# Kernel optimization log

Hardware: AMD Instinct MI355X
Metric: run time of the kernel (lower is better)

The kernel has to match this reference:

```python
import jax, jax.numpy as jnp
import numpy as np

D = 1024      # d_model
H = 16        # n_heads
DH = 64       # d_head
K = 4         # conv_kernel
C = H * DH    # channels for depthwise convs


def setup_inputs() -> dict:
    key = jax.random.key(0)
    ks = jax.random.split(key, 16)
    s = 0.02
    w = lambda k, shape: (jax.random.normal(k, shape, jnp.float32) * s)
    return {
        'hidden_states': jax.random.normal(ks[0], (4, 2048, D), jnp.float32),
        'Wq': w(ks[1], (C, D)),
        'Wk': w(ks[2], (C, D)),
        'Wv': w(ks[3], (C, D)),
        'Wa': w(ks[4], (H, D)), 'ba': jnp.zeros((H,), jnp.float32),
        'Wb': w(ks[5], (H, D)), 'bb': jnp.zeros((H,), jnp.float32),
        'conv_q_w': w(ks[6], (C, 1, K)), 'conv_q_b': jnp.zeros((C,), jnp.float32),
        'conv_k_w': w(ks[7], (C, 1, K)), 'conv_k_b': jnp.zeros((C,), jnp.float32),
        'conv_v_w': w(ks[8], (C, 1, K)), 'conv_v_b': jnp.zeros((C,), jnp.float32),
        'Wg': w(ks[9], (C, D)), 'bg': jnp.zeros((C,), jnp.float32),
        'Wo': w(ks[10], (D, C)),
    }


def _causal_conv(x, w, b):
    # x: (B, C, T); depthwise causal conv (torch pads K-1 both sides then slices [:T])
    y = jax.lax.conv_general_dilated(
        x, w, window_strides=(1,), padding=[(K - 1, 0)],
        feature_group_count=C, dimension_numbers=('NCH', 'OIH', 'NCH'))
    return y + b[None, :, None]


def reference(hidden_states, Wq, Wk, Wv, Wa, ba, Wb, bb,
              conv_q_w, conv_q_b, conv_k_w, conv_k_b, conv_v_w, conv_v_b,
              Wg, bg, Wo):
    B, T, _ = hidden_states.shape
    # projections -> (B, C, T) for conv
    q = jnp.einsum('btd,cd->bct', hidden_states, Wq)
    k = jnp.einsum('btd,cd->bct', hidden_states, Wk)
    v = jnp.einsum('btd,cd->bct', hidden_states, Wv)
    q = jax.nn.silu(_causal_conv(q, conv_q_w, conv_q_b))
    k = jax.nn.silu(_causal_conv(k, conv_k_w, conv_k_b))
    v = jax.nn.silu(_causal_conv(v, conv_v_w, conv_v_b))
    # (B, T, H, DH)
    q = q.transpose(0, 2, 1).reshape(B, T, H, DH)
    k = k.transpose(0, 2, 1).reshape(B, T, H, DH)
    v = v.transpose(0, 2, 1).reshape(B, T, H, DH)
    # F.normalize(k, p=2, dim=-1)
    k = k / jnp.maximum(jnp.linalg.norm(k, axis=-1, keepdims=True), 1e-12)
    alpha = jax.nn.sigmoid(jnp.einsum('btd,hd->bth', hidden_states, Wa) + ba)
    beta = jax.nn.sigmoid(jnp.einsum('btd,hd->bth', hidden_states, Wb) + bb)

    def step(S, xs):
        kt, vt, qt, at, bt = xs            # (B,H,DH) x3, (B,H) x2
        v_old = jnp.einsum('bhij,bhj->bhi', S, kt)
        upd = vt - at[..., None] * v_old   # (B,H,DH)
        dS = upd[..., :, None] * kt[..., None, :]
        S = jnp.clip(at[..., None, None] * S + bt[..., None, None] * dS, -5.0, 5.0)
        ot = jnp.einsum('bhij,bhj->bhi', S, qt)
        return S, ot

    S0 = jnp.zeros((B, H, DH, DH), hidden_states.dtype)
    xs = (k.transpose(1, 0, 2, 3), v.transpose(1, 0, 2, 3), q.transpose(1, 0, 2, 3),
          alpha.transpose(1, 0, 2), beta.transpose(1, 0, 2))
    _, ys = jax.lax.scan(step, S0, xs)     # ys: (T, B, H, DH)
    y = ys.transpose(1, 0, 2, 3).reshape(B, T, C)
    g = jax.nn.silu(jnp.einsum('btd,cd->btc', hidden_states, Wg) + bg)
    y = y * g
    out = jnp.einsum('btc,dc->btd', y, Wo)
    return out
```

## Files before the change

kernel.cpp:

```cpp
#include <hip/hip_runtime.h>
#include <cstdint>
#include <cstddef>

#define TSEQ 2048
#define NB   4
#define NH   16
#define MM   (NB * TSEQ)
#define KK   1024
#define NCAT 4224

typedef __attribute__((ext_vector_type(8))) __bf16 bf16x8;
typedef __attribute__((ext_vector_type(4))) float f32x4;
typedef __attribute__((ext_vector_type(4))) int   int4v;

__device__ __forceinline__ unsigned short f2bf(float f) {
  unsigned int u = __float_as_uint(f);
  u += 0x7fffu + ((u >> 16) & 1u);
  return (unsigned short)(u >> 16);
}
__device__ __forceinline__ float bf2f(unsigned short h) {
  return __uint_as_float(((unsigned int)h) << 16);
}
__device__ __forceinline__ float sigmoidf_(float x) { return 1.0f / (1.0f + expf(-x)); }
__device__ __forceinline__ float siluf_(float x)    { return x / (1.0f + expf(-x)); }

__device__ __forceinline__ uint32_t packsplit(float x) {
  unsigned short h = f2bf(x);
  unsigned short l = f2bf(x - bf2f(h));
  return ((uint32_t)h << 16) | (uint32_t)l;
}

union BF8 { bf16x8 v; unsigned short s[8]; };

__device__ __forceinline__ void frag_from_packed(const uint32_t* p, bf16x8& hi, bf16x8& lo) {
  int4v a = *(const int4v*)p;
  int4v b = *(const int4v*)(p + 4);
  BF8 H, L;
#pragma unroll
  for (int e = 0; e < 4; ++e) {
    uint32_t ua = ((const uint32_t*)&a)[e];
    uint32_t ub = ((const uint32_t*)&b)[e];
    H.s[e]     = (unsigned short)(ua >> 16);
    L.s[e]     = (unsigned short)(ua & 0xffffu);
    H.s[e + 4] = (unsigned short)(ub >> 16);
    L.s[e + 4] = (unsigned short)(ub & 0xffffu);
  }
  hi = H.v; lo = L.v;
}

__device__ __forceinline__ f32x4 mfma3(bf16x8 ah, bf16x8 al, bf16x8 bh, bf16x8 bl, f32x4 acc) {
  acc = __builtin_amdgcn_mfma_f32_16x16x32_bf16(ah, bh, acc, 0, 0, 0);
  acc = __builtin_amdgcn_mfma_f32_16x16x32_bf16(ah, bl, acc, 0, 0, 0);
  acc = __builtin_amdgcn_mfma_f32_16x16x32_bf16(al, bh, acc, 0, 0, 0);
  return acc;
}

__global__ void k_split(const float* __restrict__ x, unsigned short* __restrict__ hi,
                        unsigned short* __restrict__ lo, int n) {
  int idx = blockIdx.x * blockDim.x + threadIdx.x;
  if (idx >= n) return;
  float v = x[idx];
  unsigned short h = f2bf(v);
  hi[idx] = h;
  lo[idx] = f2bf(v - bf2f(h));
}

__global__ void k_build_wcat(const float* __restrict__ Wq, const float* __restrict__ Wk,
                             const float* __restrict__ Wv, const float* __restrict__ Wg,
                             const float* __restrict__ Wa, const float* __restrict__ Wb,
                             unsigned short* __restrict__ hi, unsigned short* __restrict__ lo) {
  int idx = blockIdx.x * blockDim.x + threadIdx.x;
  if (idx >= NCAT * KK) return;
  int row = idx >> 10, col = idx & 1023;
  float v = 0.0f;
  if      (row < 1024) v = Wq[idx];
  else if (row < 2048) v = Wk[idx - 1024 * 1024];
  else if (row < 3072) v = Wv[idx - 2048 * 1024];
  else if (row < 4096) v = Wg[idx - 3072 * 1024];
  else if (row < 4112) v = Wa[(row - 4096) * 1024 + col];
  else if (row < 4128) v = Wb[(row - 4112) * 1024 + col];
  unsigned short h = f2bf(v);
  hi[idx] = h;
  lo[idx] = f2bf(v - bf2f(h));
}

__global__ __launch_bounds__(256, 2)
void k_gemm(const unsigned short* __restrict__ Ahi, const unsigned short* __restrict__ Alo,
            const unsigned short* __restrict__ Bhi, const unsigned short* __restrict__ Blo,
            int Kdim, int mode,
            float* __restrict__ Qb, float* __restrict__ Kb, float* __restrict__ Vb,
            float* __restrict__ Gb, float* __restrict__ Ab, float* __restrict__ Bbuf,
            const float* __restrict__ bg, const float* __restrict__ ba, const float* __restrict__ bb,
            float* __restrict__ Out) {
  __shared__ __align__(16) unsigned short As_hi[128 * 32];
  __shared__ __align__(16) unsigned short As_lo[128 * 32];
  __shared__ __align__(16) unsigned short Bs_hi[128 * 32];
  __shared__ __align__(16) unsigned short Bs_lo[128 * 32];

  const int tid  = threadIdx.x;
  const int lane = tid & 63;
  const int l15  = lane & 15;
  const int quad = lane >> 4;
  const int wid  = tid >> 6;
  const int wm   = (wid >> 1) * 64;
  const int wn   = (wid & 1) * 64;
  const int m0   = blockIdx.x * 128;
  const int n0   = blockIdx.y * 128;
  const int srow = tid >> 2;
  const int skc  = (tid & 3) * 8;

  f32x4 acc[4][4];
  f32x4 zero4 = {0.f, 0.f, 0.f, 0.f};
#pragma unroll
  for (int i = 0; i < 4; ++i)
#pragma unroll
    for (int j = 0; j < 4; ++j) acc[i][j] = zero4;

  const unsigned short* pa0 = Ahi + (size_t)(m0 + srow) * Kdim + skc;
  const unsigned short* pa1 = Ahi + (size_t)(m0 + srow + 64) * Kdim + skc;
  const unsigned short* pa2 = Alo + (size_t)(m0 + srow) * Kdim + skc;
  const unsigned short* pa3 = Alo + (size_t)(m0 + srow + 64) * Kdim + skc;
  const unsigned short* pb0 = Bhi + (size_t)(n0 + srow) * Kdim + skc;
  const unsigned short* pb1 = Bhi + (size_t)(n0 + srow + 64) * Kdim + skc;
  const unsigned short* pb2 = Blo + (size_t)(n0 + srow) * Kdim + skc;
  const unsigned short* pb3 = Blo + (size_t)(n0 + srow + 64) * Kdim + skc;

  for (int kt = 0; kt < Kdim; kt += 32) {
    int4v va0 = *(const int4v*)(pa0 + kt);
    int4v va1 = *(const int4v*)(pa1 + kt);
    int4v va2 = *(const int4v*)(pa2 + kt);
    int4v va3 = *(const int4v*)(pa3 + kt);
    int4v vb0 = *(const int4v*)(pb0 + kt);
    int4v vb1 = *(const int4v*)(pb1 + kt);
    int4v vb2 = *(const int4v*)(pb2 + kt);
    int4v vb3 = *(const int4v*)(pb3 + kt);
    __syncthreads();
    *(int4v*)&As_hi[srow * 32 + skc]        = va0;
    *(int4v*)&As_hi[(srow + 64) * 32 + skc] = va1;
    *(int4v*)&As_lo[srow * 32 + skc]        = va2;
    *(int4v*)&As_lo[(srow + 64) * 32 + skc] = va3;
    *(int4v*)&Bs_hi[srow * 32 + skc]        = vb0;
    *(int4v*)&Bs_hi[(srow + 64) * 32 + skc] = vb1;
    *(int4v*)&Bs_lo[srow * 32 + skc]        = vb2;
    *(int4v*)&Bs_lo[(srow + 64) * 32 + skc] = vb3;
    __syncthreads();

    bf16x8 ah[4], al[4], bh[4], bl[4];
#pragma unroll
    for (int f = 0; f < 4; ++f) {
      int ra = (wm + f * 16 + l15) * 32 + quad * 8;
      ah[f] = *(const bf16x8*)&As_hi[ra];
      al[f] = *(const bf16x8*)&As_lo[ra];
      int rb = (wn + f * 16 + l15) * 32 + quad * 8;
      bh[f] = *(const bf16x8*)&Bs_hi[rb];
      bl[f] = *(const bf16x8*)&Bs_lo[rb];
    }
#pragma unroll
    for (int mf = 0; mf < 4; ++mf)
#pragma unroll
      for (int nf = 0; nf < 4; ++nf) {
        acc[mf][nf] = __builtin_amdgcn_mfma_f32_16x16x32_bf16(ah[mf], bh[nf], acc[mf][nf], 0, 0, 0);
        acc[mf][nf] = __builtin_amdgcn_mfma_f32_16x16x32_bf16(ah[mf], bl[nf], acc[mf][nf], 0, 0, 0);
        acc[mf][nf] = __builtin_amdgcn_mfma_f32_16x16x32_bf16(al[mf], bh[nf], acc[mf][nf], 0, 0, 0);
      }
  }

#pragma unroll
  for (int mf = 0; mf < 4; ++mf) {
    int rowb = m0 + wm + mf * 16 + quad * 4;
#pragma unroll
    for (int nf = 0; nf < 4; ++nf) {
      int col = n0 + wn + nf * 16 + l15;
      f32x4 v = acc[mf][nf];
      if (mode == 1) {
#pragma unroll
        for (int r = 0; r < 4; ++r) Out[(size_t)(rowb + r) * 1024 + col] = v[r];
      } else {
        if (col < 1024) {
#pragma unroll
          for (int r = 0; r < 4; ++r) Qb[(size_t)(rowb + r) * 1024 + col] = v[r];
        } else if (col < 2048) {
          int c = col - 1024;
#pragma unroll
          for (int r = 0; r < 4; ++r) Kb[(size_t)(rowb + r) * 1024 + c] = v[r];
        } else if (col < 3072) {
          int c = col - 2048;
#pragma unroll
          for (int r = 0; r < 4; ++r) Vb[(size_t)(rowb + r) * 1024 + c] = v[r];
        } else if (col < 4096) {
          int c = col - 3072;
          float bgc = bg[c];
#pragma unroll
          for (int r = 0; r < 4; ++r) {
            float x = v[r] + bgc;
            Gb[(size_t)(rowb + r) * 1024 + c] = siluf_(x);
          }
        } else if (col < 4112) {
          int c = col - 4096;
          float bac = ba[c];
#pragma unroll
          for (int r = 0; r < 4; ++r) Ab[(size_t)(rowb + r) * 16 + c] = sigmoidf_(v[r] + bac);
        } else if (col < 4128) {
          int c = col - 4112;
          float bbc = bb[c];
#pragma unroll
          for (int r = 0; r < 4; ++r) Bbuf[(size_t)(rowb + r) * 16 + c] = sigmoidf_(v[r] + bbc);
        }
      }
    }
  }
}

__global__ __launch_bounds__(512)
void k_intra(const float* __restrict__ Qb, const float* __restrict__ Kb,
             const float* __restrict__ Vb,
             const float* __restrict__ Ab, const float* __restrict__ Bb,
             const float* __restrict__ cqw, const float* __restrict__ cqb,
             const float* __restrict__ ckw, const float* __restrict__ ckb,
             const float* __restrict__ cvw, const float* __restrict__ cvb,
             uint32_t* __restrict__ A1buf, unsigned short* __restrict__ Qefbuf,
             unsigned short* __restrict__ G1buf, unsigned short* __restrict__ G2Tbuf,
             float* __restrict__ gCbuf) {
  __shared__ __align__(16) unsigned short Khi[64][72], Klo[64][72];
  __shared__ __align__(16) unsigned short Qhi[64][72], Qlo[64][72];
  __shared__ float Vf[64][65];
  __shared__ float Rf[64][65];
  __shared__ float Mm[64][68];
  __shared__ __align__(16) unsigned short Atthi[64][72];
  __shared__ __align__(16) uint32_t u0T[64][68], RTp[64][68];
  __shared__ __align__(16) unsigned short KwThi[64][72], KwTlo[64][72];
  __shared__ float lgs[64], gas[64], bss[64], wvs[64], ins[64];

  const int tid  = threadIdx.x;
  const int lane = tid & 63;
  const int w8   = tid >> 6;
  const int ws   = w8 & 3;
  const int hs   = w8 >> 2;
  const int l15  = lane & 15;
  const int quad = lane >> 4;
  const int bid  = blockIdx.x;
  const int c    = bid & 31;
  const int h    = (bid >> 5) & 15;
  const int b    = bid >> 9;
  const size_t ci = (size_t)bid;
  const int t0   = c * 64;
  const long rowBase = (long)b * 2048 + t0;
  const int ch   = h * 64 + lane;
  const f32x4 z4 = {0.f, 0.f, 0.f, 0.f};

  {
    long gr = (rowBase + lane) * 16 + h;
    float av = Ab[gr], bv = Bb[gr];
    float x = log2f(av);
#pragma unroll
    for (int off = 1; off < 64; off <<= 1) {
      float y = __shfl_up(x, off);
      if (lane >= off) x += y;
    }
    float l63 = __shfl(x, 63);
    lgs[lane] = x;
    gas[lane] = exp2f(x);
    bss[lane] = bv;
    wvs[lane] = exp2f(l63 - x) * bv;
  }

  {
    const float kc0 = ckw[ch * 4], kc1 = ckw[ch * 4 + 1], kc2 = ckw[ch * 4 + 2], kc3 = ckw[ch * 4 + 3], kcbv = ckb[ch];
    const float qc0 = cqw[ch * 4], qc1 = cqw[ch * 4 + 1], qc2 = cqw[ch * 4 + 2], qc3 = cqw[ch * 4 + 3], qcbv = cqb[ch];
    const float vc0 = cvw[ch * 4], vc1 = cvw[ch * 4 + 1], vc2 = cvw[ch * 4 + 2], vc3 = cvw[ch * 4 + 3], vcbv = cvb[ch];
    const int tb = t0 + w8 * 8;
    float kw0, kw1, kw2, qw0, qw1, qw2, vw0, vw1, vw2;
    {
      float kx[3], qx[3], vx[3];
#pragma unroll
      for (int d = 0; d < 3; ++d) {
        int tt = tb - 3 + d;
        float a = 0.f, bq = 0.f, cv = 0.f;
        if (tt >= 0) {
          long ro = ((long)b * 2048 + tt) * 1024 + ch;
          a = Kb[ro]; bq = Qb[ro]; cv = Vb[ro];
        }
        kx[d] = a; qx[d] = bq; vx[d] = cv;
      }
      kw0 = kx[0]; kw1 = kx[1]; kw2 = kx[2];
      qw0 = qx[0]; qw1 = qx[1]; qw2 = qx[2];
      vw0 = vx[0]; vw1 = vx[1]; vw2 = vx[2];
    }
#pragma unroll
    for (int lt = 0; lt < 8; ++lt) {
      const int s = w8 * 8 + lt;
      const long ro = (rowBase + s) * 1024 + ch;
      float kr = Kb[ro], qr = Qb[ro], vr = Vb[ro];
      float kcv = kcbv + kc0 * kw0 + kc1 * kw1 + kc2 * kw2 + kc3 * kr;
      float qcv = qcbv + qc0 * qw0 + qc1 * qw1 + qc2 * qw2 + qc3 * qr;
      float vcv = vcbv + vc0 * vw0 + vc1 * vw1 + vc2 * vw2 + vc3 * vr;
      kw0 = kw1; kw1 = kw2; kw2 = kr;
      qw0 = qw1; qw1 = qw2; qw2 = qr;
      vw0 = vw1; vw1 = vw2; vw2 = vr;
      float kv = siluf_(kcv), qv = siluf_(qcv), vv = siluf_(vcv);
      uint32_t kp_ = packsplit(kv);
      uint32_t qp_ = packsplit(qv);
      Khi[s][lane] = (unsigned short)(kp_ >> 16); Klo[s][lane] = (unsigned short)(kp_ & 0xffffu);
      Qhi[s][lane] = (unsigned short)(qp_ >> 16); Qlo[s][lane] = (unsigned short)(qp_ & 0xffffu);
      Vf[s][lane] = vv;
    }
  }
  __syncthreads();

  f32x4 accT[4];
#pragma unroll
  for (int nt = 0; nt < 4; ++nt) accT[nt] = z4;
#pragma unroll
  for (int ks = 0; ks < 2; ++ks) {
    bf16x8 ah, al;
    if (hs == 0) {
      ah = *(const bf16x8*)&Khi[ws * 16 + l15][ks * 32 + quad * 8];
      al = *(const bf16x8*)&Klo[ws * 16 + l15][ks * 32 + quad * 8];
    } else {
      ah = *(const bf16x8*)&Qhi[ws * 16 + l15][ks * 32 + quad * 8];
      al = *(const bf16x8*)&Qlo[ws * 16 + l15][ks * 32 + quad * 8];
    }
#pragma unroll
    for (int nt = 0; nt < 4; ++nt) {
      bf16x8 bh = *(const bf16x8*)&Khi[nt * 16 + l15][ks * 32 + quad * 8];
      bf16x8 bl = *(const bf16x8*)&Klo[nt * 16 + l15][ks * 32 + quad * 8];
      accT[nt] = mfma3(ah, al, bh, bl, accT[nt]);
    }
  }
  if (hs == 0) {
#pragma unroll
    for (int nt = 0; nt < 4; ++nt)
      if (nt == ws) {
#pragma unroll
        for (int r = 0; r < 4; ++r)
          if (l15 == quad * 4 + r) ins[nt * 16 + l15] = rsqrtf(fmaxf(accT[nt][r], 1e-24f));
      }
  }
  __syncthreads();

  {
    if (hs == 0) {
#pragma unroll
      for (int nt = 0; nt < 4; ++nt) {
        int sc = nt * 16 + l15;
        float insc = ins[sc], lgc = lgs[sc], bsc = bss[sc];
#pragma unroll
        for (int r = 0; r < 4; ++r) {
          int sr = ws * 16 + quad * 4 + r;
          Mm[sr][sc] = (sc < sr) ? exp2f(lgs[sr] - lgc) * bsc * ins[sr] * insc * accT[nt][r] : 0.f;
        }
      }
    } else {
#pragma unroll
      for (int nt = 0; nt < 4; ++nt) {
        int sc = nt * 16 + l15;
        float insc = ins[sc], lgc = lgs[sc], bsc = bss[sc];
#pragma unroll
        for (int r = 0; r < 4; ++r) {
          int sr = ws * 16 + quad * 4 + r;
          Atthi[sr][sc] = f2bf((sc <= sr) ? exp2f(lgs[sr] - lgc) * bsc * insc * accT[nt][r] : 0.f);
        }
      }
    }
    int s = w8 * 8 + (lane & 7);
    int jb = (lane >> 3) * 8;
    float rsc = gas[s] * ins[s];
    float wsc = wvs[s] * ins[s];
    BF8 H0, L0;
    H0.v = *(const bf16x8*)&Khi[s][jb];
    L0.v = *(const bf16x8*)&Klo[s][jb];
#pragma unroll
    for (int e = 0; e < 8; ++e) {
      float kv = bf2f(H0.s[e]) + bf2f(L0.s[e]);
      Rf[s][jb + e] = kv * rsc;
      uint32_t p0 = packsplit(kv * wsc);
      KwThi[jb + e][s] = (unsigned short)(p0 >> 16);
      KwTlo[jb + e][s] = (unsigned short)(p0 & 0xffffu);
    }
  }
  if (tid == 0) gCbuf[ci] = gas[63];
  __syncthreads();

  if (w8 < 2) {
    float* RHS = (w8 == 0) ? &Vf[0][0] : &Rf[0][0];
    const int i = lane;
    float u[64];
#pragma unroll
    for (int d = 0; d < 4; ++d) {
      const int base = d * 16;
#pragma unroll
      for (int r2 = 0; r2 < 16; ++r2) {
        const int s = base + r2;
        float acc = RHS[s * 65 + i];
#pragma unroll
        for (int r = 0; r < r2; ++r) acc = fmaf(-Mm[s][base + r], u[base + r], acc);
        u[s] = acc;
        RHS[s * 65 + i] = acc;
      }
      if (d < 3) {
#pragma unroll 1
        for (int s = base + 16; s < 64; ++s) {
          f32x4 m0 = *(const f32x4*)&Mm[s][base];
          f32x4 m1 = *(const f32x4*)&Mm[s][base + 4];
          f32x4 m2 = *(const f32x4*)&Mm[s][base + 8];
          f32x4 m3 = *(const f32x4*)&Mm[s][base + 12];
          float a0 = m0[0] * u[base + 0] + m0[1] * u[base + 1] + m0[2] * u[base + 2] + m0[3] * u[base + 3];
          float a1 = m1[0] * u[base + 4] + m1[1] * u[base + 5] + m1[2] * u[base + 6] + m1[3] * u[base + 7];
          float a2 = m2[0] * u[base + 8] + m2[1] * u[base + 9] + m2[2] * u[base + 10] + m2[3] * u[base + 11];
          float a3 = m3[0] * u[base + 12] + m3[1] * u[base + 13] + m3[2] * u[base + 14] + m3[3] * u[base + 15];
          RHS[s * 65 + i] = RHS[s * 65 + i] - ((a0 + a1) + (a2 + a3));
        }
      }
    }
  }
  __syncthreads();

#pragma unroll
  for (int r = 0; r < 8; ++r) {
    int i = w8 * 8 + r;
    u0T[i][lane] = packsplit(Vf[lane][i]);
    RTp[i][lane] = packsplit(Rf[lane][i]);
  }
  __syncthreads();

  if (hs == 0) {
    {
      f32x4 acc[4];
#pragma unroll
      for (int nt = 0; nt < 4; ++nt) acc[nt] = z4;
#pragma unroll
      for (int ks = 0; ks < 2; ++ks) {
        bf16x8 ta = *(const bf16x8*)&Atthi[ws * 16 + l15][ks * 32 + quad * 8];
#pragma unroll
        for (int nt = 0; nt < 4; ++nt) {
          bf16x8 uh, ul;
          frag_from_packed(&u0T[nt * 16 + l15][ks * 32 + quad * 8], uh, ul);
          acc[nt] = __builtin_amdgcn_mfma_f32_16x16x32_bf16(ta, uh, acc[nt], 0, 0, 0);
          acc[nt] = __builtin_amdgcn_mfma_f32_16x16x32_bf16(ta, ul, acc[nt], 0, 0, 0);
        }
      }
#pragma unroll
      for (int nt = 0; nt < 4; ++nt)
#pragma unroll
        for (int r = 0; r < 4; ++r) {
          int t = ws * 16 + quad * 4 + r, i = nt * 16 + l15;
          A1buf[ci * 4096 + t * 64 + i] = packsplit(acc[nt][r]);
        }
    }
    {
      f32x4 acc[4];
#pragma unroll
      for (int nt = 0; nt < 4; ++nt) acc[nt] = z4;
#pragma unroll
      for (int ks = 0; ks < 2; ++ks) {
        bf16x8 ta = *(const bf16x8*)&Atthi[ws * 16 + l15][ks * 32 + quad * 8];
#pragma unroll
        for (int nt = 0; nt < 4; ++nt) {
          bf16x8 rh, rl;
          frag_from_packed(&RTp[nt * 16 + l15][ks * 32 + quad * 8], rh, rl);
          acc[nt] = __builtin_amdgcn_mfma_f32_16x16x32_bf16(ta, rh, acc[nt], 0, 0, 0);
          acc[nt] = __builtin_amdgcn_mfma_f32_16x16x32_bf16(ta, rl, acc[nt], 0, 0, 0);
        }
      }
#pragma unroll
      for (int nt = 0; nt < 4; ++nt)
#pragma unroll
        for (int r = 0; r < 4; ++r) {
          int t = ws * 16 + quad * 4 + r, j = nt * 16 + l15;
          float q = bf2f(Qhi[t][j]) + bf2f(Qlo[t][j]);
          Qefbuf[ci * 4096 + t * 64 + j] = f2bf(gas[t] * q - acc[nt][r]);
        }
    }
  } else {
    {
      f32x4 acc[4];
#pragma unroll
      for (int nt = 0; nt < 4; ++nt) acc[nt] = z4;
#pragma unroll
      for (int ks = 0; ks < 2; ++ks) {
        bf16x8 uh, ul;
        frag_from_packed(&u0T[ws * 16 + l15][ks * 32 + quad * 8], uh, ul);
#pragma unroll
        for (int nt = 0; nt < 4; ++nt) {
          bf16x8 kh = *(const bf16x8*)&KwThi[nt * 16 + l15][ks * 32 + quad * 8];
          bf16x8 kl = *(const bf16x8*)&KwTlo[nt * 16 + l15][ks * 32 + quad * 8];
          acc[nt] = mfma3(uh, ul, kh, kl, acc[nt]);
        }
      }
#pragma unroll
      for (int nt = 0; nt < 4; ++nt)
#pragma unroll
        for (int r = 0; r < 4; ++r) {
          int i = ws * 16 + quad * 4 + r, j = nt * 16 + l15;
          G1buf[ci * 4096 + i * 64 + j] = f2bf(acc[nt][r]);
        }
    }
    {
      f32x4 acc[4];
#pragma unroll
      for (int nt = 0; nt < 4; ++nt) acc[nt] = z4;
#pragma unroll
      for (int ks = 0; ks < 2; ++ks) {
        bf16x8 rh, rl;
        frag_from_packed(&RTp[ws * 16 + l15][ks * 32 + quad * 8], rh, rl);
#pragma unroll
        for (int nt = 0; nt < 4; ++nt) {
          bf16x8 kh = *(const bf16x8*)&KwThi[nt * 16 + l15][ks * 32 + quad * 8];
          bf16x8 kl = *(const bf16x8*)&KwTlo[nt * 16 + l15][ks * 32 + quad * 8];
          acc[nt] = mfma3(rh, rl, kh, kl, acc[nt]);
        }
      }
#pragma unroll
      for (int nt = 0; nt < 4; ++nt) {
        int j = nt * 16 + l15;
        int mb = ws * 16 + quad * 4;
        uint32_t lo32 = (uint32_t)f2bf(acc[nt][0]) | ((uint32_t)f2bf(acc[nt][1]) << 16);
        uint32_t hi32 = (uint32_t)f2bf(acc[nt][2]) | ((uint32_t)f2bf(acc[nt][3]) << 16);
        uint32_t* dst = (uint32_t*)&G2Tbuf[ci * 4096 + j * 64 + mb];
        dst[0] = lo32; dst[1] = hi32;
      }
    }
  }
}

__global__ __launch_bounds__(256)
void k_serial(const uint32_t* __restrict__ A1buf, const unsigned short* __restrict__ Qefbuf,
              const unsigned short* __restrict__ G1buf, const unsigned short* __restrict__ G2Tbuf,
              const float* __restrict__ gCbuf, const float* __restrict__ Gb,
              unsigned short* __restrict__ Yhi, unsigned short* __restrict__ Ylo) {
  __shared__ __align__(16) unsigned short QefL[64][72], G2TL[64][72];
  __shared__ __align__(16) unsigned short S0hi[16][72], S0lo[16][72];

  const int tid  = threadIdx.x;
  const int lane = tid & 63;
  const int w    = tid >> 6;
  const int l15  = lane & 15;
  const int quad = lane >> 4;
  const int bh   = blockIdx.x >> 2;
  const int iq   = blockIdx.x & 3;
  const int ibase = iq * 16;
  const int b    = bh >> 4;
  const int h    = bh & 15;
  const f32x4 z4 = {0.f, 0.f, 0.f, 0.f};

  for (int n = tid; n < 16 * 72; n += 256) { (&S0hi[0][0])[n] = 0; (&S0lo[0][0])[n] = 0; }

  float s0[4] = {0.f, 0.f, 0.f, 0.f};

  const int qRow0 = tid >> 3, qCol = (tid & 7) * 8;
  const int qRow1 = (tid + 256) >> 3;
  int4v rQv[2], rG2v[2];
  uint32_t rA[4];
  unsigned short rG1[4];
  float pg[4], pgC;
  {
    const uint32_t* pA  = A1buf + (size_t)bh * 32 * 4096;
    const uint32_t* pQ  = (const uint32_t*)Qefbuf + (size_t)bh * 32 * 2048;
    const unsigned short* pG1 = G1buf + (size_t)bh * 32 * 4096;
    const uint32_t* pG2 = (const uint32_t*)G2Tbuf + (size_t)bh * 32 * 2048;
    rQv[0]  = *(const int4v*)&pQ[tid * 4];
    rQv[1]  = *(const int4v*)&pQ[(tid + 256) * 4];
    rG2v[0] = *(const int4v*)&pG2[tid * 4];
    rG2v[1] = *(const int4v*)&pG2[(tid + 256) * 4];
#pragma unroll
    for (int r = 0; r < 4; ++r) {
      rA[r]  = pA[(w * 16 + quad * 4 + r) * 64 + ibase + l15];
      rG1[r] = pG1[(ibase + quad * 4 + r) * 64 + w * 16 + l15];
      pg[r]  = Gb[((long)b * 2048 + w * 16 + quad * 4 + r) * 1024 + h * 64 + ibase + l15];
    }
    pgC = gCbuf[(size_t)bh * 32];
  }
  __syncthreads();

#pragma unroll 1
  for (int c = 0; c < 32; ++c) {
    *(int4v*)&QefL[qRow0][qCol] = rQv[0];
    *(int4v*)&QefL[qRow1][qCol] = rQv[1];
    *(int4v*)&G2TL[qRow0][qCol] = rG2v[0];
    *(int4v*)&G2TL[qRow1][qCol] = rG2v[1];
    uint32_t a1l[4]; unsigned short g1l[4]; float pgl[4];
#pragma unroll
    for (int e = 0; e < 4; ++e) { a1l[e] = rA[e]; g1l[e] = rG1[e]; pgl[e] = pg[e]; }
    float gC = pgC;
    __syncthreads();

    f32x4 accO = z4, accS = z4;
#pragma unroll
    for (int ks = 0; ks < 2; ++ks) {
      bf16x8 qa  = *(const bf16x8*)&QefL[w * 16 + l15][ks * 32 + quad * 8];
      bf16x8 sh0 = *(const bf16x8*)&S0hi[l15][ks * 32 + quad * 8];
      bf16x8 sl0 = *(const bf16x8*)&S0lo[l15][ks * 32 + quad * 8];
      accO = __builtin_amdgcn_mfma_f32_16x16x32_bf16(qa, sh0, accO, 0, 0, 0);
      accO = __builtin_amdgcn_mfma_f32_16x16x32_bf16(qa, sl0, accO, 0, 0, 0);
      bf16x8 g2 = *(const bf16x8*)&G2TL[w * 16 + l15][ks * 32 + quad * 8];
      accS = __builtin_amdgcn_mfma_f32_16x16x32_bf16(sh0, g2, accS, 0, 0, 0);
      accS = __builtin_amdgcn_mfma_f32_16x16x32_bf16(sl0, g2, accS, 0, 0, 0);
    }
    {
      const int cc = (c + 1 < 32) ? c + 1 : 31;
      const uint32_t* pA  = A1buf + ((size_t)bh * 32 + cc) * 4096;
      const uint32_t* pQ  = (const uint32_t*)Qefbuf + ((size_t)bh * 32 + cc) * 2048;
      const unsigned short* pG1 = G1buf + ((size_t)bh * 32 + cc) * 4096;
      const uint32_t* pG2 = (const uint32_t*)G2Tbuf + ((size_t)bh * 32 + cc) * 2048;
      rQv[0]  = *(const int4v*)&pQ[tid * 4];
      rQv[1]  = *(const int4v*)&pQ[(tid + 256) * 4];
      rG2v[0] = *(const int4v*)&pG2[tid * 4];
      rG2v[1] = *(const int4v*)&pG2[(tid + 256) * 4];
#pragma unroll
      for (int r = 0; r < 4; ++r) {
        rA[r]  = pA[(w * 16 + quad * 4 + r) * 64 + ibase + l15];
        rG1[r] = pG1[(ibase + quad * 4 + r) * 64 + w * 16 + l15];
        pg[r]  = Gb[((long)b * 2048 + cc * 64 + w * 16 + quad * 4 + r) * 1024 + h * 64 + ibase + l15];
      }
      pgC = gCbuf[(size_t)bh * 32 + cc];
    }
    __syncthreads();

#pragma unroll
    for (int r = 0; r < 4; ++r) {
      int t = w * 16 + quad * 4 + r;
      float o = accO[r] + bf2f((unsigned short)(a1l[r] >> 16)) + bf2f((unsigned short)(a1l[r] & 0xffffu));
      float y = o * pgl[r];
      long ro = ((long)b * 2048 + c * 64 + t) * 1024 + h * 64 + ibase + l15;
      unsigned short hy = f2bf(y);
      Yhi[ro] = hy;
      Ylo[ro] = f2bf(y - bf2f(hy));
    }
#pragma unroll
    for (int r = 0; r < 4; ++r) {
      int i = quad * 4 + r, j = w * 16 + l15;
      float sn = gC * s0[r] + bf2f(g1l[r]) - accS[r];
      s0[r] = sn;
      uint32_t p = packsplit(sn);
      S0hi[i][j] = (unsigned short)(p >> 16);
      S0lo[i][j] = (unsigned short)(p & 0xffffu);
    }
  }
}

extern "C" void kernel_launch(void* const* d_in, const int* in_sizes, int n_in,
                              void* d_out, int out_size, void* d_ws, size_t ws_size,
                              hipStream_t stream) {
  const float* X   = (const float*)d_in[0];
  const float* Wq  = (const float*)d_in[1];
  const float* Wk  = (const float*)d_in[2];
  const float* Wv  = (const float*)d_in[3];
  const float* Wa  = (const float*)d_in[4];
  const float* ba  = (const float*)d_in[5];
  const float* Wb  = (const float*)d_in[6];
  const float* bb  = (const float*)d_in[7];
  const float* cqw = (const float*)d_in[8];
  const float* cqb = (const float*)d_in[9];
  const float* ckw = (const float*)d_in[10];
  const float* ckb = (const float*)d_in[11];
  const float* cvw = (const float*)d_in[12];
  const float* cvb = (const float*)d_in[13];
  const float* Wg  = (const float*)d_in[14];
  const float* bg  = (const float*)d_in[15];
  const float* Wo  = (const float*)d_in[16];
  float* Out = (float*)d_out;

  char* ws = (char*)d_ws;
  size_t off = 0;
  auto alloc = [&](size_t bytes) -> void* {
    void* p = ws + off;
    off += (bytes + 255) & ~(size_t)255;
    return p;
  };
  unsigned short* Xhi = (unsigned short*)alloc((size_t)MM * KK * 2);
  unsigned short* Xlo = (unsigned short*)alloc((size_t)MM * KK * 2);
  unsigned short* Whi = (unsigned short*)alloc((size_t)NCAT * KK * 2);
  unsigned short* Wlo = (unsigned short*)alloc((size_t)NCAT * KK * 2);
  float* Qb  = (float*)alloc((size_t)MM * 1024 * 4);
  float* Kb  = (float*)alloc((size_t)MM * 1024 * 4);
  float* Vb  = (float*)alloc((size_t)MM * 1024 * 4);
  float* Ab  = (float*)alloc((size_t)MM * 16 * 4);
  float* Bbf = (float*)alloc((size_t)MM * 16 * 4);
  uint32_t*       A1buf  = (uint32_t*)alloc((size_t)2048 * 4096 * 4);
  unsigned short* G1buf  = (unsigned short*)alloc((size_t)2048 * 4096 * 2);
  unsigned short* G2Tbuf = (unsigned short*)alloc((size_t)2048 * 4096 * 2);
  float*          gCbuf  = (float*)alloc((size_t)2048 * 4);
  float* Gb = Out;
  unsigned short* Yhi = Xhi;
  unsigned short* Ylo = Xlo;
  unsigned short* Qefbuf = Whi;
  unsigned short* Wohi = Whi;
  unsigned short* Wolo = Wlo;

  const int nX = MM * KK;
  k_split<<<(nX + 255) / 256, 256, 0, stream>>>(X, Xhi, Xlo, nX);
  k_build_wcat<<<(NCAT * KK + 255) / 256, 256, 0, stream>>>(Wq, Wk, Wv, Wg, Wa, Wb, Whi, Wlo);
  k_gemm<<<dim3(MM / 128, NCAT / 128), 256, 0, stream>>>(
      Xhi, Xlo, Whi, Wlo, KK, 0, Qb, Kb, Vb, Gb, Ab, Bbf, bg, ba, bb, nullptr);
  k_intra<<<NB * NH * 32, 512, 0, stream>>>(Qb, Kb, Vb, Ab, Bbf,
                                            cqw, cqb, ckw, ckb, cvw, cvb,
                                            A1buf, Qefbuf, G1buf, G2Tbuf, gCbuf);
  k_serial<<<NB * NH * 4, 256, 0, stream>>>(A1buf, Qefbuf, G1buf, G2Tbuf, gCbuf, Gb, Yhi, Ylo);
  k_split<<<(1024 * 1024 + 255) / 256, 256, 0, stream>>>(Wo, Wohi, Wolo, 1024 * 1024);
  k_gemm<<<dim3(MM / 128, 1024 / 128), 256, 0, stream>>>(
      Yhi, Ylo, Wohi, Wolo, KK, 1, nullptr, nullptr, nullptr, nullptr, nullptr, nullptr,
      nullptr, nullptr, nullptr, Out);
}
```

Baseline: 639.5 us.

## Make intra-chunk kernel persistent over eight chunks with register-prefetched loads

k_intra now launches 256 blocks instead of 2048, and each block loops over eight consecutive 64-step chunks of one (batch, head). At the start of each chunk, the gate scan and conv/SiLU inputs are computed into registers before a barrier, then written to shared memory, so global loads can run while the previous chunk's shared buffers are still in use. This saves per-block setup such as the conv weight loads, but cuts the grid to 256 blocks, which leaves much less parallelism and occupancy for latency hiding on a GPU with many CUs.

```diff
diff --git a/kernel.cpp b/kernel.cpp
--- a/kernel.cpp
+++ b/kernel.cpp
@@ -239,285 +239,297 @@
   const int l15  = lane & 15;
   const int quad = lane >> 4;
   const int bid  = blockIdx.x;
-  const int c    = bid & 31;
-  const int h    = (bid >> 5) & 15;
-  const int b    = bid >> 9;
-  const size_t ci = (size_t)bid;
-  const int t0   = c * 64;
-  const long rowBase = (long)b * 2048 + t0;
+  const int cg   = bid & 3;
+  const int h    = (bid >> 2) & 15;
+  const int b    = bid >> 6;
   const int ch   = h * 64 + lane;
   const f32x4 z4 = {0.f, 0.f, 0.f, 0.f};
 
-  {
-    long gr = (rowBase + lane) * 16 + h;
-    float av = Ab[gr], bv = Bb[gr];
-    float x = log2f(av);
-#pragma unroll
-    for (int off = 1; off < 64; off <<= 1) {
-      float y = __shfl_up(x, off);
-      if (lane >= off) x += y;
-    }
-    float l63 = __shfl(x, 63);
-    lgs[lane] = x;
-    gas[lane] = exp2f(x);
-    bss[lane] = bv;
-    wvs[lane] = exp2f(l63 - x) * bv;
-  }
-
-  {
-    const float kc0 = ckw[ch * 4], kc1 = ckw[ch * 4 + 1], kc2 = ckw[ch * 4 + 2], kc3 = ckw[ch * 4 + 3], kcbv = ckb[ch];
-    const float qc0 = cqw[ch * 4], qc1 = cqw[ch * 4 + 1], qc2 = cqw[ch * 4 + 2], qc3 = cqw[ch * 4 + 3], qcbv = cqb[ch];
-    const float vc0 = cvw[ch * 4], vc1 = cvw[ch * 4 + 1], vc2 = cvw[ch * 4 + 2], vc3 = cvw[ch * 4 + 3], vcbv = cvb[ch];
-    const int tb = t0 + w8 * 8;
-    float kw0, kw1, kw2, qw0, qw1, qw2, vw0, vw1, vw2;
+  const float kc0 = ckw[ch * 4], kc1 = ckw[ch * 4 + 1], kc2 = ckw[ch * 4 + 2], kc3 = ckw[ch * 4 + 3], kcbv = ckb[ch];
+  const float qc0 = cqw[ch * 4], qc1 = cqw[ch * 4 + 1], qc2 = cqw[ch * 4 + 2], qc3 = cqw[ch * 4 + 3], qcbv = cqb[ch];
+  const float vc0 = cvw[ch * 4], vc1 = cvw[ch * 4 + 1], vc2 = cvw[ch * 4 + 2], vc3 = cvw[ch * 4 + 3], vcbv = cvb[ch];
+
+#pragma unroll 1
+  for (int ic = 0; ic < 8; ++ic) {
+    const int c    = cg * 8 + ic;
+    const size_t ci = (size_t)((b * 16 + h) * 32 + c);
+    const int t0   = c * 64;
+    const long rowBase = (long)b * 2048 + t0;
+
+    float gx, g_gas, g_bss, g_wvs;
     {
-      float kx[3], qx[3], vx[3];
-#pragma unroll
-      for (int d = 0; d < 3; ++d) {
-        int tt = tb - 3 + d;
-        float a = 0.f, bq = 0.f, cv = 0.f;
-        if (tt >= 0) {
-          long ro = ((long)b * 2048 + tt) * 1024 + ch;
-          a = Kb[ro]; bq = Qb[ro]; cv = Vb[ro];
-        }
-        kx[d] = a; qx[d] = bq; vx[d] = cv;
-      }
-      kw0 = kx[0]; kw1 = kx[1]; kw2 = kx[2];
-      qw0 = qx[0]; qw1 = qx[1]; qw2 = qx[2];
-      vw0 = vx[0]; vw1 = vx[1]; vw2 = vx[2];
-    }
+      long gr = (rowBase + lane) * 16 + h;
+      float avv = Ab[gr], bvv = Bb[gr];
+      float x = log2f(avv);
+#pragma unroll
+      for (int off = 1; off < 64; off <<= 1) {
+        float y = __shfl_up(x, off);
+        if (lane >= off) x += y;
+      }
+      float l63 = __shfl(x, 63);
+      gx = x; g_gas = exp2f(x); g_bss = bvv; g_wvs = exp2f(l63 - x) * bvv;
+    }
+    uint32_t kp[8], qp[8];
+    float vvv[8];
+    {
+      const int tb = t0 + w8 * 8;
+      float kw0, kw1, kw2, qw0, qw1, qw2, vw0, vw1, vw2;
+      {
+        float kx[3], qx[3], vx[3];
+#pragma unroll
+        for (int d = 0; d < 3; ++d) {
+          int tt = tb - 3 + d;
+          float a = 0.f, bq = 0.f, cv = 0.f;
+          if (tt >= 0) {
+            long ro = ((long)b * 2048 + tt) * 1024 + ch;
+            a = Kb[ro]; bq = Qb[ro]; cv = Vb[ro];
+          }
+          kx[d] = a; qx[d] = bq; vx[d] = cv;
+        }
+        kw0 = kx[0]; kw1 = kx[1]; kw2 = kx[2];
+        qw0 = qx[0]; qw1 = qx[1]; qw2 = qx[2];
+        vw0 = vx[0]; vw1 = vx[1]; vw2 = vx[2];
+      }
+#pragma unroll
+      for (int lt = 0; lt < 8; ++lt) {
+        const int s = w8 * 8 + lt;
+        const long ro = (rowBase + s) * 1024 + ch;
+        float kr = Kb[ro], qr = Qb[ro], vr = Vb[ro];
+        float kcv = kcbv + kc0 * kw0 + kc1 * kw1 + kc2 * kw2 + kc3 * kr;
+        float qcv = qcbv + qc0 * qw0 + qc1 * qw1 + qc2 * qw2 + qc3 * qr;
+        float vcv = vcbv + vc0 * vw0 + vc1 * vw1 + vc2 * vw2 + vc3 * vr;
+        kw0 = kw1; kw1 = kw2; kw2 = kr;
+        qw0 = qw1; qw1 = qw2; qw2 = qr;
+        vw0 = vw1; vw1 = vw2; vw2 = vr;
+        kp[lt] = packsplit(siluf_(kcv));
+        qp[lt] = packsplit(siluf_(qcv));
+        vvv[lt] = siluf_(vcv);
+      }
+    }
+    __syncthreads();
+
+    lgs[lane] = gx; gas[lane] = g_gas; bss[lane] = g_bss; wvs[lane] = g_wvs;
 #pragma unroll
     for (int lt = 0; lt < 8; ++lt) {
       const int s = w8 * 8 + lt;
-      const long ro = (rowBase + s) * 1024 + ch;
-      float kr = Kb[ro], qr = Qb[ro], vr = Vb[ro];
-      float kcv = kcbv + kc0 * kw0 + kc1 * kw1 + kc2 * kw2 + kc3 * kr;
-      float qcv = qcbv + qc0 * qw0 + qc1 * qw1 + qc2 * qw2 + qc3 * qr;
-      float vcv = vcbv + vc0 * vw0 + vc1 * vw1 + vc2 * vw2 + vc3 * vr;
-      kw0 = kw1; kw1 = kw2; kw2 = kr;
-      qw0 = qw1; qw1 = qw2; qw2 = qr;
-      vw0 = vw1; vw1 = vw2; vw2 = vr;
-      float kv = siluf_(kcv), qv = siluf_(qcv), vv = siluf_(vcv);
-      uint32_t kp_ = packsplit(kv);
-      uint32_t qp_ = packsplit(qv);
-      Khi[s][lane] = (unsigned short)(kp_ >> 16); Klo[s][lane] = (unsigned short)(kp_ & 0xffffu);
-      Qhi[s][lane] = (unsigned short)(qp_ >> 16); Qlo[s][lane] = (unsigned short)(qp_ & 0xffffu);
-      Vf[s][lane] = vv;
-    }
-  }
-  __syncthreads();
-
-  f32x4 accT[4];
-#pragma unroll
-  for (int nt = 0; nt < 4; ++nt) accT[nt] = z4;
-#pragma unroll
-  for (int ks = 0; ks < 2; ++ks) {
-    bf16x8 ah, al;
+      Khi[s][lane] = (unsigned short)(kp[lt] >> 16); Klo[s][lane] = (unsigned short)(kp[lt] & 0xffffu);
+      Qhi[s][lane] = (unsigned short)(qp[lt] >> 16); Qlo[s][lane] = (unsigned short)(qp[lt] & 0xffffu);
+      Vf[s][lane] = vvv[lt];
+    }
+    __syncthreads();
+
+    f32x4 accT[4];
+#pragma unroll
+    for (int nt = 0; nt < 4; ++nt) accT[nt] = z4;
+#pragma unroll
+    for (int ks = 0; ks < 2; ++ks) {
+      bf16x8 ah, al;
+      if (hs == 0) {
+        ah = *(const bf16x8*)&Khi[ws * 16 + l15][ks * 32 + quad * 8];
+        al = *(const bf16x8*)&Klo[ws * 16 + l15][ks * 32 + quad * 8];
+      } else {
+        ah = *(const bf16x8*)&Qhi[ws * 16 + l15][ks * 32 + quad * 8];
+        al = *(const bf16x8*)&Qlo[ws * 16 + l15][ks * 32 + quad * 8];
+      }
+#pragma unroll
+      for (int nt = 0; nt < 4; ++nt) {
+        bf16x8 bh = *(const bf16x8*)&Khi[nt * 16 + l15][ks * 32 + quad * 8];
+        bf16x8 bl = *(const bf16x8*)&Klo[nt * 16 + l15][ks * 32 + quad * 8];
+        accT[nt] = mfma3(ah, al, bh, bl, accT[nt]);
+      }
+    }
     if (hs == 0) {
-      ah = *(const bf16x8*)&Khi[ws * 16 + l15][ks * 32 + quad * 8];
-      al = *(const bf16x8*)&Klo[ws * 16 + l15][ks * 32 + quad * 8];
+#pragma unroll
+      for (int nt = 0; nt < 4; ++nt)
+        if (nt == ws) {
+#pragma unroll
+          for (int r = 0; r < 4; ++r)
+            if (l15 == quad * 4 + r) ins[nt * 16 + l15] = rsqrtf(fmaxf(accT[nt][r], 1e-24f));
+        }
+    }
+    __syncthreads();
+
+    {
+      if (hs == 0) {
+#pragma unroll
+        for (int nt = 0; nt < 4; ++nt) {
+          int sc = nt * 16 + l15;
+          float insc = ins[sc], lgc = lgs[sc], bsc = bss[sc];
+#pragma unroll
+          for (int r = 0; r < 4; ++r) {
+            int sr = ws * 16 + quad * 4 + r;
+            Mm[sr][sc] = (sc < sr) ? exp2f(lgs[sr] - lgc) * bsc * ins[sr] * insc * accT[nt][r] : 0.f;
+          }
+        }
+      } else {
+#pragma unroll
+        for (int nt = 0; nt < 4; ++nt) {
+          int sc = nt * 16 + l15;
+          float insc = ins[sc], lgc = lgs[sc], bsc = bss[sc];
+#pragma unroll
+          for (int r = 0; r < 4; ++r) {
+            int sr = ws * 16 + quad * 4 + r;
+            Atthi[sr][sc] = f2bf((sc <= sr) ? exp2f(lgs[sr] - lgc) * bsc * insc * accT[nt][r] : 0.f);
+          }
+        }
+      }
+      int s = w8 * 8 + (lane & 7);
+      int jb = (lane >> 3) * 8;
+      float rsc = gas[s] * ins[s];
+      float wsc = wvs[s] * ins[s];
+      BF8 H0, L0;
+      H0.v = *(const bf16x8*)&Khi[s][jb];
+      L0.v = *(const bf16x8*)&Klo[s][jb];
+#pragma unroll
+      for (int e = 0; e < 8; ++e) {
+        float kv = bf2f(H0.s[e]) + bf2f(L0.s[e]);
+        Rf[s][jb + e] = kv * rsc;
+        uint32_t p0 = packsplit(kv * wsc);
+        KwThi[jb + e][s] = (unsigned short)(p0 >> 16);
+        KwTlo[jb + e][s] = (unsigned short)(p0 & 0xffffu);
+      }
+    }
+    if (tid == 0) gCbuf[ci] = gas[63];
+    __syncthreads();
+
+    if (w8 < 2) {
+      float* RHS = (w8 == 0) ? &Vf[0][0] : &Rf[0][0];
+      const int i = lane;
+      float u[64];
+#pragma unroll
+      for (int d = 0; d < 4; ++d) {
+        const int base = d * 16;
+#pragma unroll
+        for (int r2 = 0; r2 < 16; ++r2) {
+          const int s = base + r2;
+          float acc = RHS[s * 65 + i];
+#pragma unroll
+          for (int r = 0; r < r2; ++r) acc = fmaf(-Mm[s][base + r], u[base + r], acc);
+          u[s] = acc;
+          RHS[s * 65 + i] = acc;
+        }
+        if (d < 3) {
+#pragma unroll 1
+          for (int s = base + 16; s < 64; ++s) {
+            f32x4 m0 = *(const f32x4*)&Mm[s][base];
+            f32x4 m1 = *(const f32x4*)&Mm[s][base + 4];
+            f32x4 m2 = *(const f32x4*)&Mm[s][base + 8];
+            f32x4 m3 = *(const f32x4*)&Mm[s][base + 12];
+            float a0 = m0[0] * u[base + 0] + m0[1] * u[base + 1] + m0[2] * u[base + 2] + m0[3] * u[base + 3];
+            float a1 = m1[0] * u[base + 4] + m1[1] * u[base + 5] + m1[2] * u[base + 6] + m1[3] * u[base + 7];
+            float a2 = m2[0] * u[base + 8] + m2[1] * u[base + 9] + m2[2] * u[base + 10] + m2[3] * u[base + 11];
+            float a3 = m3[0] * u[base + 12] + m3[1] * u[base + 13] + m3[2] * u[base + 14] + m3[3] * u[base + 15];
+            RHS[s * 65 + i] = RHS[s * 65 + i] - ((a0 + a1) + (a2 + a3));
+          }
+        }
+      }
+    }
+    __syncthreads();
+
+#pragma unroll
+    for (int r = 0; r < 8; ++r) {
+      int i = w8 * 8 + r;
+      u0T[i][lane] = packsplit(Vf[lane][i]);
+      RTp[i][lane] = packsplit(Rf[lane][i]);
+    }
+    __syncthreads();
+
+    if (hs == 0) {
+      {
+        f32x4 acc[4];
+#pragma unroll
+        for (int nt = 0; nt < 4; ++nt) acc[nt] = z4;
+#pragma unroll
+        for (int ks = 0; ks < 2; ++ks) {
+          bf16x8 ta = *(const bf16x8*)&Atthi[ws * 16 + l15][ks * 32 + quad * 8];
+#pragma unroll
+          for (int nt = 0; nt < 4; ++nt) {
+            bf16x8 uh, ul;
+            frag_from_packed(&u0T[nt * 16 + l15][ks * 32 + quad * 8], uh, ul);
+            acc[nt] = __builtin_amdgcn_mfma_f32_16x16x32_bf16(ta, uh, acc[nt], 0, 0, 0);
+            acc[nt] = __builtin_amdgcn_mfma_f32_16x16x32_bf16(ta, ul, acc[nt], 0, 0, 0);
+          }
+        }
+#pragma unroll
+        for (int nt = 0; nt < 4; ++nt)
+#pragma unroll
+          for (int r = 0; r < 4; ++r) {
+            int t = ws * 16 + quad * 4 + r, i = nt * 16 + l15;
+            A1buf[ci * 4096 + t * 64 + i] = packsplit(acc[nt][r]);
+          }
+      }
+      {
+        f32x4 acc[4];
+#pragma unroll
+        for (int nt = 0; nt < 4; ++nt) acc[nt] = z4;
+#pragma unroll
+        for (int ks = 0; ks < 2; ++ks) {
+          bf16x8 ta = *(const bf16x8*)&Atthi[ws * 16 + l15][ks * 32 + quad * 8];
+#pragma unroll
+          for (int nt = 0; nt < 4; ++nt) {
+            bf16x8 rh, rl;
+            frag_from_packed(&RTp[nt * 16 + l15][ks * 32 + quad * 8], rh, rl);
+            acc[nt] = __builtin_amdgcn_mfma_f32_16x16x32_bf16(ta, rh, acc[nt], 0, 0, 0);
+            acc[nt] = __builtin_amdgcn_mfma_f32_16x16x32_bf16(ta, rl, acc[nt], 0, 0, 0);
+          }
+        }
+#pragma unroll
+        for (int nt = 0; nt < 4; ++nt)
+#pragma unroll
+          for (int r = 0; r < 4; ++r) {
+            int t = ws * 16 + quad * 4 + r, j = nt * 16 + l15;
+            float q = bf2f(Qhi[t][j]) + bf2f(Qlo[t][j]);
+            Qefbuf[ci * 4096 + t * 64 + j] = f2bf(gas[t] * q - acc[nt][r]);
+          }
+      }
     } else {
-      ah = *(const bf16x8*)&Qhi[ws * 16 + l15][ks * 32 + quad * 8];
-      al = *(const bf16x8*)&Qlo[ws * 16 + l15][ks * 32 + quad * 8];
-    }
-#pragma unroll
-    for (int nt = 0; nt < 4; ++nt) {
-      bf16x8 bh = *(const bf16x8*)&Khi[nt * 16 + l15][ks * 32 + quad * 8];
-      bf16x8 bl = *(const bf16x8*)&Klo[nt * 16 + l15][ks * 32 + quad * 8];
-      accT[nt] = mfma3(ah, al, bh, bl, accT[nt]);
-    }
-  }
-  if (hs == 0) {
-#pragma unroll
-    for (int nt = 0; nt < 4; ++nt)
-      if (nt == ws) {
-#pragma unroll
-        for (int r = 0; r < 4; ++r)
-          if (l15 == quad * 4 + r) ins[nt * 16 + l15] = rsqrtf(fmaxf(accT[nt][r], 1e-24f));
-      }
-  }
-  __syncthreads();
-
-  {
-    if (hs == 0) {
-#pragma unroll
-      for (int nt = 0; nt < 4; ++nt) {
-        int sc = nt * 16 + l15;
-        float insc = ins[sc], lgc = lgs[sc], bsc = bss[sc];
-#pragma unroll
-        for (int r = 0; r < 4; ++r) {
-          int sr = ws * 16 + quad * 4 + r;
-          Mm[sr][sc] = (sc < sr) ? exp2f(lgs[sr] - lgc) * bsc * ins[sr] * insc * accT[nt][r] : 0.f;
-        }
-      }
-    } else {
-#pragma unroll
-      for (int nt = 0; nt < 4; ++nt) {
-        int sc = nt * 16 + l15;
-        float insc = ins[sc], lgc = lgs[sc], bsc = bss[sc];
-#pragma unroll
-        for (int r = 0; r < 4; ++r) {
-          int sr = ws * 16 + quad * 4 + r;
-          Atthi[sr][sc] = f2bf((sc <= sr) ? exp2f(lgs[sr] - lgc) * bsc * insc * accT[nt][r] : 0.f);
-        }
-      }
-    }
-    int s = w8 * 8 + (lane & 7);
-    int jb = (lane >> 3) * 8;
-    float rsc = gas[s] * ins[s];
-    float wsc = wvs[s] * ins[s];
-    BF8 H0, L0;
-    H0.v = *(const bf16x8*)&Khi[s][jb];
-    L0.v = *(const bf16x8*)&Klo[s][jb];
-#pragma unroll
-    for (int e = 0; e < 8; ++e) {
-      float kv = bf2f(H0.s[e]) + bf2f(L0.s[e]);
-      Rf[s][jb + e] = kv * rsc;
-      uint32_t p0 = packsplit(kv * wsc);
-      KwThi[jb + e][s] = (unsigned short)(p0 >> 16);
-      KwTlo[jb + e][s] = (unsigned short)(p0 & 0xffffu);
-    }
-  }
-  if (tid == 0) gCbuf[ci] = gas[63];
-  __syncthreads();
-
-  if (w8 < 2) {
-    float* RHS = (w8 == 0) ? &Vf[0][0] : &Rf[0][0];
-    const int i = lane;
-    float u[64];
-#pragma unroll
-    for (int d = 0; d < 4; ++d) {
-      const int base = d * 16;
-#pragma unroll
-      for (int r2 = 0; r2 < 16; ++r2) {
-        const int s = base + r2;
-        float acc = RHS[s * 65 + i];
-#pragma unroll
-        for (int r = 0; r < r2; ++r) acc = fmaf(-Mm[s][base + r], u[base + r], acc);
-        u[s] = acc;
-        RHS[s * 65 + i] = acc;
-      }
-      if (d < 3) {
-#pragma unroll 1
-        for (int s = base + 16; s < 64; ++s) {
-          f32x4 m0 = *(const f32x4*)&Mm[s][base];
-          f32x4 m1 = *(const f32x4*)&Mm[s][base + 4];
-          f32x4 m2 = *(const f32x4*)&Mm[s][base + 8];
-          f32x4 m3 = *(const f32x4*)&Mm[s][base + 12];
-          float a0 = m0[0] * u[base + 0] + m0[1] * u[base + 1] + m0[2] * u[base + 2] + m0[3] * u[base + 3];
-          float a1 = m1[0] * u[base + 4] + m1[1] * u[base + 5] + m1[2] * u[base + 6] + m1[3] * u[base + 7];
-          float a2 = m2[0] * u[base + 8] + m2[1] * u[base + 9] + m2[2] * u[base + 10] + m2[3] * u[base + 11];
-          float a3 = m3[0] * u[base + 12] + m3[1] * u[base + 13] + m3[2] * u[base + 14] + m3[3] * u[base + 15];
-          RHS[s * 65 + i] = RHS[s * 65 + i] - ((a0 + a1) + (a2 + a3));
-        }
-      }
-    }
-  }
-  __syncthreads();
-
-#pragma unroll
-  for (int r = 0; r < 8; ++r) {
-    int i = w8 * 8 + r;
-    u0T[i][lane] = packsplit(Vf[lane][i]);
-    RTp[i][lane] = packsplit(Rf[lane][i]);
-  }
-  __syncthreads();
-
-  if (hs == 0) {
-    {
-      f32x4 acc[4];
-#pragma unroll
-      for (int nt = 0; nt < 4; ++nt) acc[nt] = z4;
-#pragma unroll
-      for (int ks = 0; ks < 2; ++ks) {
-        bf16x8 ta = *(const bf16x8*)&Atthi[ws * 16 + l15][ks * 32 + quad * 8];
+      {
+        f32x4 acc[4];
+#pragma unroll
+        for (int nt = 0; nt < 4; ++nt) acc[nt] = z4;
+#pragma unroll
+        for (int ks = 0; ks < 2; ++ks) {
+          bf16x8 uh, ul;
+          frag_from_packed(&u0T[ws * 16 + l15][ks * 32 + quad * 8], uh, ul);
+#pragma unroll
+          for (int nt = 0; nt < 4; ++nt) {
+            bf16x8 kh = *(const bf16x8*)&KwThi[nt * 16 + l15][ks * 32 + quad * 8];
+            bf16x8 kl = *(const bf16x8*)&KwTlo[nt * 16 + l15][ks * 32 + quad * 8];
+            acc[nt] = mfma3(uh, ul, kh, kl, acc[nt]);
+          }
+        }
+#pragma unroll
+        for (int nt = 0; nt < 4; ++nt)
+#pragma unroll
+          for (int r = 0; r < 4; ++r) {
+            int i = ws * 16 + quad * 4 + r, j = nt * 16 + l15;
+            G1buf[ci * 4096 + i * 64 + j] = f2bf(acc[nt][r]);
+          }
+      }
+      {
+        f32x4 acc[4];
+#pragma unroll
+        for (int nt = 0; nt < 4; ++nt) acc[nt] = z4;
+#pragma unroll
+        for (int ks = 0; ks < 2; ++ks) {
+          bf16x8 rh, rl;
+          frag_from_packed(&RTp[ws * 16 + l15][ks * 32 + quad * 8], rh, rl);
+#pragma unroll
+          for (int nt = 0; nt < 4; ++nt) {
+            bf16x8 kh = *(const bf16x8*)&KwThi[nt * 16 + l15][ks * 32 + quad * 8];
+            bf16x8 kl = *(const bf16x8*)&KwTlo[nt * 16 + l15][ks * 32 + quad * 8];
+            acc[nt] = mfma3(rh, rl, kh, kl, acc[nt]);
+          }
+        }
 #pragma unroll
         for (int nt = 0; nt < 4; ++nt) {
-          bf16x8 uh, ul;
-          frag_from_packed(&u0T[nt * 16 + l15][ks * 32 + quad * 8], uh, ul);
-          acc[nt] = __builtin_amdgcn_mfma_f32_16x16x32_bf16(ta, uh, acc[nt], 0, 0, 0);
-          acc[nt] = __builtin_amdgcn_mfma_f32_16x16x32_bf16(ta, ul, acc[nt], 0, 0, 0);
-        }
-      }
-#pragma unroll
-      for (int nt = 0; nt < 4; ++nt)
-#pragma unroll
-        for (int r = 0; r < 4; ++r) {
-          int t = ws * 16 + quad * 4 + r, i = nt * 16 + l15;
-          A1buf[ci * 4096 + t * 64 + i] = packsplit(acc[nt][r]);
-        }
-    }
-    {
-      f32x4 acc[4];
-#pragma unroll
-      for (int nt = 0; nt < 4; ++nt) acc[nt] = z4;
-#pragma unroll
-      for (int ks = 0; ks < 2; ++ks) {
-        bf16x8 ta = *(const bf16x8*)&Atthi[ws * 16 + l15][ks * 32 + quad * 8];
-#pragma unroll
-        for (int nt = 0; nt < 4; ++nt) {
-          bf16x8 rh, rl;
-          frag_from_packed(&RTp[nt * 16 + l15][ks * 32 + quad * 8], rh, rl);
-          acc[nt] = __builtin_amdgcn_mfma_f32_16x16x32_bf16(ta, rh, acc[nt], 0, 0, 0);
-          acc[nt] = __builtin_amdgcn_mfma_f32_16x16x32_bf16(ta, rl, acc[nt], 0, 0, 0);
-        }
-      }
-#pragma unroll
-      for (int nt = 0; nt < 4; ++nt)
-#pragma unroll
-        for (int r = 0; r < 4; ++r) {
-          int t = ws * 16 + quad * 4 + r, j = nt * 16 + l15;
-          float q = bf2f(Qhi[t][j]) + bf2f(Qlo[t][j]);
-          Qefbuf[ci * 4096 + t * 64 + j] = f2bf(gas[t] * q - acc[nt][r]);
-        }
-    }
-  } else {
-    {
-      f32x4 acc[4];
-#pragma unroll
-      for (int nt = 0; nt < 4; ++nt) acc[nt] = z4;
-#pragma unroll
-      for (int ks = 0; ks < 2; ++ks) {
-        bf16x8 uh, ul;
-        frag_from_packed(&u0T[ws * 16 + l15][ks * 32 + quad * 8], uh, ul);
-#pragma unroll
-        for (int nt = 0; nt < 4; ++nt) {
-          bf16x8 kh = *(const bf16x8*)&KwThi[nt * 16 + l15][ks * 32 + quad * 8];
-          bf16x8 kl = *(const bf16x8*)&KwTlo[nt * 16 + l15][ks * 32 + quad * 8];
-          acc[nt] = mfma3(uh, ul, kh, kl, acc[nt]);
-        }
-      }
-#pragma unroll
-      for (int nt = 0; nt < 4; ++nt)
-#pragma unroll
-        for (int r = 0; r < 4; ++r) {
-          int i = ws * 16 + quad * 4 + r, j = nt * 16 + l15;
-          G1buf[ci * 4096 + i * 64 + j] = f2bf(acc[nt][r]);
-        }
-    }
-    {
-      f32x4 acc[4];
-#pragma unroll
-      for (int nt = 0; nt < 4; ++nt) acc[nt] = z4;
-#pragma unroll
-      for (int ks = 0; ks < 2; ++ks) {
-        bf16x8 rh, rl;
-        frag_from_packed(&RTp[ws * 16 + l15][ks * 32 + quad * 8], rh, rl);
-#pragma unroll
-        for (int nt = 0; nt < 4; ++nt) {
-          bf16x8 kh = *(const bf16x8*)&KwThi[nt * 16 + l15][ks * 32 + quad * 8];
-          bf16x8 kl = *(const bf16x8*)&KwTlo[nt * 16 + l15][ks * 32 + quad * 8];
-          acc[nt] = mfma3(rh, rl, kh, kl, acc[nt]);
-        }
-      }
-#pragma unroll
-      for (int nt = 0; nt < 4; ++nt) {
-        int j = nt * 16 + l15;
-        int mb = ws * 16 + quad * 4;
-        uint32_t lo32 = (uint32_t)f2bf(acc[nt][0]) | ((uint32_t)f2bf(acc[nt][1]) << 16);
-        uint32_t hi32 = (uint32_t)f2bf(acc[nt][2]) | ((uint32_t)f2bf(acc[nt][3]) << 16);
-        uint32_t* dst = (uint32_t*)&G2Tbuf[ci * 4096 + j * 64 + mb];
-        dst[0] = lo32; dst[1] = hi32;
+          int j = nt * 16 + l15;
+          int mb = ws * 16 + quad * 4;
+          uint32_t lo32 = (uint32_t)f2bf(acc[nt][0]) | ((uint32_t)f2bf(acc[nt][1]) << 16);
+          uint32_t hi32 = (uint32_t)f2bf(acc[nt][2]) | ((uint32_t)f2bf(acc[nt][3]) << 16);
+          uint32_t* dst = (uint32_t*)&G2Tbuf[ci * 4096 + j * 64 + mb];
+          dst[0] = lo32; dst[1] = hi32;
+        }
       }
     }
   }
@@ -692,9 +704,9 @@
   k_build_wcat<<<(NCAT * KK + 255) / 256, 256, 0, stream>>>(Wq, Wk, Wv, Wg, Wa, Wb, Whi, Wlo);
   k_gemm<<<dim3(MM / 128, NCAT / 128), 256, 0, stream>>>(
       Xhi, Xlo, Whi, Wlo, KK, 0, Qb, Kb, Vb, Gb, Ab, Bbf, bg, ba, bb, nullptr);
-  k_intra<<<NB * NH * 32, 512, 0, stream>>>(Qb, Kb, Vb, Ab, Bbf,
-                                            cqw, cqb, ckw, ckb, cvw, cvb,
-                                            A1buf, Qefbuf, G1buf, G2Tbuf, gCbuf);
+  k_intra<<<NB * NH * 4, 512, 0, stream>>>(Qb, Kb, Vb, Ab, Bbf,
+                                           cqw, cqb, ckw, ckb, cvw, cvb,
+                                           A1buf, Qefbuf, G1buf, G2Tbuf, gCbuf);
   k_serial<<<NB * NH * 4, 256, 0, stream>>>(A1buf, Qefbuf, G1buf, G2Tbuf, gCbuf, Gb, Yhi, Ylo);
   k_split<<<(1024 * 1024 + 255) / 256, 256, 0, stream>>>(Wo, Wohi, Wolo, 1024 * 1024);
   k_gemm<<<dim3(MM / 128, 1024 / 128), 256, 0, stream>>>(
```

Result: slower. 656.2 us (+2.6%).
